# Kernel tuning notes

Hardware: AMD Instinct MI355X
Metric: run time of the kernel (lower is better)

The kernel has to match this reference:

```python
import jax, jax.numpy as jnp
import numpy as np

N = 6144          # number_of_nodes
E = 196608        # random edges (self-loops appended in reference, as add_self_loops does)
L_GAT = 10        # GAT num_layers
NEG_SLOPE = 0.2   # GATConv leaky_relu slope


def setup_inputs() -> dict:
    key = jax.random.key(0)
    ks = jax.random.split(key, 27)
    g = lambda i, shape, s=0.3: jax.random.normal(ks[i], shape, jnp.float32) * s
    return {
        "x": jax.random.normal(ks[0], (N, 3), jnp.float32),
        "mask": jax.random.uniform(ks[1], (N,), dtype=jnp.float32),
        "edge_index": jax.random.randint(ks[2], (2, E), 0, N),
        # 10-layer GAT (heads=1): per-layer lin weight, att_src, att_dst, bias
        "gat_W": g(3, (L_GAT, 3, 3)), "gat_asrc": g(4, (L_GAT, 3)),
        "gat_adst": g(5, (L_GAT, 3)), "gat_b": g(6, (L_GAT, 3), 0.1),
        # nn.MultiheadAttention(embed_dim=3, num_heads=3)
        "mha_in_w": g(7, (9, 3)), "mha_in_b": g(8, (9,), 0.1),
        "mha_out_w": g(9, (3, 3)), "mha_out_b": g(10, (3,), 0.1),
        # TransformerConv(3, 3, heads=1)
        "tc_Wq": g(11, (3, 3)), "tc_bq": g(12, (3,), 0.1),
        "tc_Wk": g(13, (3, 3)), "tc_bk": g(14, (3,), 0.1),
        "tc_Wv": g(15, (3, 3)), "tc_bv": g(16, (3,), 0.1),
        "tc_Wskip": g(17, (3, 3)), "tc_bskip": g(18, (3,), 0.1),
        # actor MLP: Linear(3N,16) -> ReLU -> Linear(16,32) -> ReLU -> Linear(32,N)
        "mlp_W1": g(19, (3 * N, 16), 0.02), "mlp_b1": g(20, (16,), 0.1),
        "mlp_W2": g(21, (16, 32), 0.2), "mlp_b2": g(22, (32,), 0.1),
        "mlp_W3": g(23, (32, N), 0.2), "mlp_b3": jnp.zeros((N,), jnp.float32),
        # critic Linear(1,1)
        "critic_W": g(24, (1, 1)), "critic_b": g(25, (1,), 0.1),
    }


def _seg_softmax(e, seg, n):
    # numerically-stable softmax grouped by destination node
    m = jax.lax.stop_gradient(jax.ops.segment_max(e, seg, num_segments=n))
    w = jnp.exp(e - m[seg])
    z = jax.ops.segment_sum(w, seg, num_segments=n)
    return w / (z[seg] + 1e-16)


def reference(x, mask, edge_index, gat_W, gat_asrc, gat_adst, gat_b,
              mha_in_w, mha_in_b, mha_out_w, mha_out_b,
              tc_Wq, tc_bq, tc_Wk, tc_bk, tc_Wv, tc_bv, tc_Wskip, tc_bskip,
              mlp_W1, mlp_b1, mlp_W2, mlp_b2, mlp_W3, mlp_b3,
              critic_W, critic_b):
    n = x.shape[0]
    loops = jnp.arange(n)
    src = jnp.concatenate([edge_index[0], loops])  # add_self_loops
    dst = jnp.concatenate([edge_index[1], loops])

    # ---- 10-layer GAT (heads=1, ReLU between layers) ----
    h = x
    for l in range(L_GAT):
        xp = h @ gat_W[l]                                   # [N,3]
        e = jax.nn.leaky_relu(xp[src] @ gat_asrc[l] + xp[dst] @ gat_adst[l], NEG_SLOPE)
        alpha = _seg_softmax(e, dst, n)
        h_new = jax.ops.segment_sum(alpha[:, None] * xp[src], dst, num_segments=n) + gat_b[l]
        h = jax.nn.relu(h_new) if l < L_GAT - 1 else h_new

    # ---- MultiheadAttention(embed_dim=3, num_heads=3 => head_dim=1), history = [h] ----
    qkv = h @ mha_in_w.T + mha_in_b                         # [N,9]
    q, k, v = qkv[:, 0:3], qkv[:, 3:6], qkv[:, 6:9]
    scores = jnp.einsum('nh,mh->hnm', q, k)                 # head_dim=1 -> scale = 1
    attn = jax.nn.softmax(scores, axis=-1)                  # [3,N,N] -- dominant memory
    o = jnp.einsum('hnm,mh->nh', attn, v)                   # [N,3]
    h2 = o @ mha_out_w.T + mha_out_b

    # ---- TransformerConv(3, 3, heads=1) ----
    q2 = h2 @ tc_Wq + tc_bq
    k2 = h2 @ tc_Wk + tc_bk
    v2 = h2 @ tc_Wv + tc_bv
    logit = (q2[dst] * k2[src]).sum(-1) * (1.0 / np.sqrt(3.0))
    alpha2 = _seg_softmax(logit, dst, n)
    agg = jax.ops.segment_sum(alpha2[:, None] * v2[src], dst, num_segments=n)
    h3 = agg + h2 @ tc_Wskip + tc_bskip                     # root_weight skip

    # ---- actor MLP over flattened node features ----
    flat = h3.reshape(-1)                                   # [3N]
    a1 = jax.nn.relu(flat @ mlp_W1 + mlp_b1)
    a2 = jax.nn.relu(a1 @ mlp_W2 + mlp_b2)
    results = (a2 @ mlp_W3 + mlp_b3)[:, None]               # [N,1]

    new_results = results[:, 0] * mask
    value = jnp.mean(results @ critic_W + critic_b)
    return new_results, value
```

## Files before the change

kernel.cpp:

```cpp
#include <hip/hip_runtime.h>

#define N 6144
#define E 196608
#define EN (E + N)
#define LGAT 10
#define HBLK 198
#define GBLK 384
#define MCH 192

typedef unsigned int u32;

__device__ __forceinline__ u32 f2key(float f) {
    u32 u = __float_as_uint(f);
    return (u & 0x80000000u) ? ~u : (u | 0x80000000u);
}
__device__ __forceinline__ float key2f(u32 k) {
    u32 u = (k & 0x80000000u) ? (k & 0x7FFFFFFFu) : ~k;
    return __uint_as_float(u);
}
__device__ __forceinline__ float aload_f(const float* p2) {
    return __hip_atomic_load(p2, __ATOMIC_RELAXED, __HIP_MEMORY_SCOPE_AGENT);
}
__device__ __forceinline__ u32 aload_u(const u32* p2) {
    return __hip_atomic_load(p2, __ATOMIC_RELAXED, __HIP_MEMORY_SCOPE_AGENT);
}

struct P {
    const float *x, *mask, *gat_W, *gat_asrc, *gat_adst, *gat_b;
    const float *in_w, *in_b, *out_w, *out_b;
    const float *Wq, *bq, *Wk, *bk, *Wv, *bv, *Wsk, *bsk;
    const float *W1, *b1, *W2, *b2, *W3, *b3, *cW, *cb;
    const int *src, *dst;
    float4 *nodeA, *nodeB;
    float *sdstA, *sdstB;
    float *qkv, *q2, *h2, *h3, *part;
    float4 *kv2;
    float *a1pre, *a2buf, *sumres;
    u32 *deg, *offs, *cursor, *kmaxk, *kmink;
    u32 *kmaxk2, *kmink2;
    u32 *ssmaxk;
    u32 *ctr;
    int *ssorted;
    float *out;
};

__global__ void k_init(P p) {
    int t = blockIdx.x * 256 + threadIdx.x;
    p.deg[t] = 0u;
    if (t < 16) p.a1pre[t] = 0.f;
    else if (t == 16) p.sumres[0] = 0.f;
    else if (t >= 32 && t < 35) { p.kmaxk[t - 32] = 0u; p.kmink[t - 32] = 0xFFFFFFFFu; }
    else if (t >= 35 && t < 38) { p.kmaxk2[t - 35] = 0u; p.kmink2[t - 35] = 0xFFFFFFFFu; }
    else if (t >= 48 && t < 48 + LGAT) p.ssmaxk[t - 48] = 0u;
    else if (t >= 64 && t < 72) p.ctr[t - 64] = 0u;
}

__global__ void k_hist(P p) {
    __shared__ u32 spart[256];
    __shared__ bool last;
    int t = blockIdx.x * 256 + threadIdx.x;
    #pragma unroll
    for (int k = 0; k < 4; ++k) {
        int e = t + k * (HBLK * 256);
        int d = (e < E) ? p.dst[e] : (e - E);
        atomicAdd(&p.deg[d], 1u);
    }
    __syncthreads();
    if (threadIdx.x == 0) {
        __threadfence();
        last = (atomicAdd(&p.ctr[0], 1u) == HBLK - 1);
    }
    __syncthreads();
    if (!last) return;
    int tid = threadIdx.x;
    u32 loc[24];
    u32 sum = 0;
    #pragma unroll
    for (int i = 0; i < 24; ++i) { loc[i] = sum; sum += aload_u(&p.deg[tid * 24 + i]); }
    spart[tid] = sum;
    __syncthreads();
    for (int o = 1; o < 256; o <<= 1) {
        u32 v = (tid >= o) ? spart[tid - o] : 0u;
        __syncthreads();
        spart[tid] += v;
        __syncthreads();
    }
    u32 base = (tid == 0) ? 0u : spart[tid - 1];
    #pragma unroll
    for (int i = 0; i < 24; ++i) {
        u32 off = base + loc[i];
        p.offs[tid * 24 + i] = off;
        p.cursor[tid * 24 + i] = off;
    }
    if (tid == 255) p.offs[N] = spart[255];
}

__global__ void k_scatter(P p) {
    int t = blockIdx.x * 256 + threadIdx.x;
    #pragma unroll
    for (int k = 0; k < 4; ++k) {
        int e = t + k * (HBLK * 256);
        int s = (e < E) ? p.src[e] : (e - E);
        int d = (e < E) ? p.dst[e] : (e - E);
        u32 pos = atomicAdd(&p.cursor[d], 1u);
        p.ssorted[pos] = s;
    }
    if (t < N) {
        float h0 = p.x[t * 3 + 0], h1 = p.x[t * 3 + 1], h2 = p.x[t * 3 + 2];
        const float* W = p.gat_W;
        float xp0 = h0 * W[0] + h1 * W[3] + h2 * W[6];
        float xp1 = h0 * W[1] + h1 * W[4] + h2 * W[7];
        float xp2 = h0 * W[2] + h1 * W[5] + h2 * W[8];
        float ss = xp0 * p.gat_asrc[0] + xp1 * p.gat_asrc[1] + xp2 * p.gat_asrc[2];
        p.nodeA[t] = make_float4(xp0, xp1, xp2, ss);
        p.sdstA[t] = xp0 * p.gat_adst[0] + xp1 * p.gat_adst[1] + xp2 * p.gat_adst[2];
        float m = ss;
        #pragma unroll
        for (int o = 32; o; o >>= 1) m = fmaxf(m, __shfl_xor(m, o));
        if ((threadIdx.x & 63) == 0) atomicMax(&p.ssmaxk[0], f2key(m));
    }
}

__global__ __launch_bounds__(256) void k_gat(P p, const float4* __restrict__ nin,
                                             const float* __restrict__ sdin,
                                             float4* __restrict__ nout,
                                             float* __restrict__ sdout, int l) {
    __shared__ float ssh[16];
    __shared__ float kksh[16][3];
    int gid = blockIdx.x * 256 + threadIdx.x;
    int d = gid >> 4;
    int lane = gid & 15;
    int tid = threadIdx.x;
    u32 beg = p.offs[d], end = p.offs[d + 1];
    float sd = sdin[d];
    float vb = key2f(p.ssmaxk[l]) + sd;
    float M = (vb >= 0.f) ? vb : 0.2f * vb;
    float sz = 0.f, s0 = 0.f, s1 = 0.f, s2 = 0.f;
    for (u32 i = beg + lane; i < end; i += 16) {
        float4 r = nin[p.ssorted[i]];
        float v = r.w + sd;
        v = (v >= 0.f) ? v : 0.2f * v;
        float w = __expf(v - M);
        sz += w; s0 += w * r.x; s1 += w * r.y; s2 += w * r.z;
    }
    #pragma unroll
    for (int o = 1; o < 16; o <<= 1) {
        sz += __shfl_xor(sz, o);
        s0 += __shfl_xor(s0, o);
        s1 += __shfl_xor(s1, o);
        s2 += __shfl_xor(s2, o);
    }
    if (lane == 0) {
        float z = sz + 1e-16f;
        float o0 = s0 / z + p.gat_b[l * 3 + 0];
        float o1 = s1 / z + p.gat_b[l * 3 + 1];
        float o2 = s2 / z + p.gat_b[l * 3 + 2];
        if (l < LGAT - 1) {
            o0 = fmaxf(o0, 0.f); o1 = fmaxf(o1, 0.f); o2 = fmaxf(o2, 0.f);
            const float* W = p.gat_W + (l + 1) * 9;
            float xp0 = o0 * W[0] + o1 * W[3] + o2 * W[6];
            float xp1 = o0 * W[1] + o1 * W[4] + o2 * W[7];
            float xp2 = o0 * W[2] + o1 * W[5] + o2 * W[8];
            const float* as = p.gat_asrc + (l + 1) * 3;
            const float* ad = p.gat_adst + (l + 1) * 3;
            float ss = xp0 * as[0] + xp1 * as[1] + xp2 * as[2];
            nout[d] = make_float4(xp0, xp1, xp2, ss);
            sdout[d] = xp0 * ad[0] + xp1 * ad[1] + xp2 * ad[2];
            ssh[tid >> 4] = ss;
        } else {
            float kk[9];
            #pragma unroll
            for (int j = 0; j < 9; ++j) {
                kk[j] = o0 * p.in_w[j * 3 + 0] + o1 * p.in_w[j * 3 + 1] +
                        o2 * p.in_w[j * 3 + 2] + p.in_b[j];
                p.qkv[d * 9 + j] = kk[j];
            }
            kksh[tid >> 4][0] = kk[3];
            kksh[tid >> 4][1] = kk[4];
            kksh[tid >> 4][2] = kk[5];
        }
    }
    __syncthreads();
    if (l < LGAT - 1) {
        if (tid == 0) {
            float m = ssh[0];
            #pragma unroll
            for (int j = 1; j < 16; ++j) m = fmaxf(m, ssh[j]);
            atomicMax(&p.ssmaxk[l + 1], f2key(m));
        }
    } else {
        if (tid < 3) {
            float mx = -1e30f, mn = 1e30f;
            #pragma unroll
            for (int g = 0; g < 16; ++g) {
                mx = fmaxf(mx, kksh[g][tid]);
                mn = fminf(mn, kksh[g][tid]);
            }
            atomicMax(&p.kmaxk[tid], f2key(mx));
            atomicMin(&p.kmink[tid], f2key(mn));
        }
    }
}

__global__ void k_att_partial(P p) {
    __shared__ float4 kvA[MCH];
    __shared__ float2 kvB[MCH];
    int tid = threadIdx.x;
    int chunk = blockIdx.y;
    int mbase = chunk * MCH;
    for (int mm = tid; mm < MCH; mm += 256) {
        const float* qk = p.qkv + (size_t)(mbase + mm) * 9;
        kvA[mm] = make_float4(qk[3], qk[4], qk[5], qk[6]);
        kvB[mm] = make_float2(qk[7], qk[8]);
    }
    __syncthreads();
    int n = blockIdx.x * 256 + tid;
    float q0 = p.qkv[n * 9 + 0], q1 = p.qkv[n * 9 + 1], q2 = p.qkv[n * 9 + 2];
    float kmx0 = key2f(p.kmaxk[0]), kmx1 = key2f(p.kmaxk[1]), kmx2 = key2f(p.kmaxk[2]);
    float kmn0 = key2f(p.kmink[0]), kmn1 = key2f(p.kmink[1]), kmn2 = key2f(p.kmink[2]);
    float M0 = (q0 >= 0.f) ? q0 * kmx0 : q0 * kmn0;
    float M1 = (q1 >= 0.f) ? q1 * kmx1 : q1 * kmn1;
    float M2 = (q2 >= 0.f) ? q2 * kmx2 : q2 * kmn2;
    float num0 = 0, den0 = 0, num1 = 0, den1 = 0, num2 = 0, den2 = 0;
    #pragma unroll 4
    for (int mm = 0; mm < MCH; ++mm) {
        float4 a = kvA[mm];
        float2 b = kvB[mm];
        float t0 = __expf(q0 * a.x - M0); den0 += t0; num0 += t0 * a.w;
        float t1 = __expf(q1 * a.y - M1); den1 += t1; num1 += t1 * b.x;
        float t2 = __expf(q2 * a.z - M2); den2 += t2; num2 += t2 * b.y;
    }
    float* pp = p.part + (size_t)chunk * 6 * N + n;
    pp[0] = num0; pp[N] = den0; pp[2 * N] = num1;
    pp[3 * N] = den1; pp[4 * N] = num2; pp[5 * N] = den2;
}

__global__ void k_att_reduce(P p) {
    int n = blockIdx.x * 256 + threadIdx.x;
    float num[3] = {0.f, 0.f, 0.f}, den[3] = {0.f, 0.f, 0.f};
    for (int c = 0; c < 32; ++c) {
        const float* pp = p.part + (size_t)c * 6 * N + n;
        #pragma unroll
        for (int hh = 0; hh < 3; ++hh) {
            num[hh] += pp[hh * 2 * N];
            den[hh] += pp[(hh * 2 + 1) * N];
        }
    }
    float o[3];
    #pragma unroll
    for (int hh = 0; hh < 3; ++hh) o[hh] = num[hh] / den[hh];
    float h2v[3];
    #pragma unroll
    for (int c = 0; c < 3; ++c) {
        h2v[c] = p.out_b[c] + o[0] * p.out_w[c * 3 + 0] +
                 o[1] * p.out_w[c * 3 + 1] + o[2] * p.out_w[c * 3 + 2];
        p.h2[n * 3 + c] = h2v[c];
    }
    float q2v[3], k2v[3], v2v[3];
    #pragma unroll
    for (int c = 0; c < 3; ++c) {
        q2v[c] = p.bq[c] + h2v[0] * p.Wq[c] + h2v[1] * p.Wq[3 + c] + h2v[2] * p.Wq[6 + c];
        k2v[c] = p.bk[c] + h2v[0] * p.Wk[c] + h2v[1] * p.Wk[3 + c] + h2v[2] * p.Wk[6 + c];
        v2v[c] = p.bv[c] + h2v[0] * p.Wv[c] + h2v[1] * p.Wv[3 + c] + h2v[2] * p.Wv[6 + c];
        p.q2[n * 3 + c] = q2v[c];
    }
    p.kv2[n * 2 + 0] = make_float4(k2v[0], k2v[1], k2v[2], v2v[0]);
    p.kv2[n * 2 + 1] = make_float4(v2v[1], v2v[2], 0.f, 0.f);
    #pragma unroll
    for (int hh = 0; hh < 3; ++hh) {
        float mx = k2v[hh], mn = k2v[hh];
        #pragma unroll
        for (int o2 = 32; o2; o2 >>= 1) {
            mx = fmaxf(mx, __shfl_xor(mx, o2));
            mn = fminf(mn, __shfl_xor(mn, o2));
        }
        if ((threadIdx.x & 63) == 0) {
            atomicMax(&p.kmaxk2[hh], f2key(mx));
            atomicMin(&p.kmink2[hh], f2key(mn));
        }
    }
}

__global__ __launch_bounds__(256) void k_tc_edge(P p) {
    int gid = blockIdx.x * 256 + threadIdx.x;
    int d = gid >> 4;
    int lane = gid & 15;
    u32 beg = p.offs[d], end = p.offs[d + 1];
    float q0 = p.q2[d * 3 + 0], q1 = p.q2[d * 3 + 1], q2 = p.q2[d * 3 + 2];
    const float RS3 = 0.57735026919f;
    float kx0 = key2f(p.kmaxk2[0]), kx1 = key2f(p.kmaxk2[1]), kx2 = key2f(p.kmaxk2[2]);
    float kn0 = key2f(p.kmink2[0]), kn1 = key2f(p.kmink2[1]), kn2 = key2f(p.kmink2[2]);
    float M = ((q0 >= 0.f ? q0 * kx0 : q0 * kn0) +
               (q1 >= 0.f ? q1 * kx1 : q1 * kn1) +
               (q2 >= 0.f ? q2 * kx2 : q2 * kn2)) * RS3;
    float sz = 0.f, s0 = 0.f, s1 = 0.f, s2 = 0.f;
    for (u32 i = beg + lane; i < end; i += 16) {
        int s = p.ssorted[i];
        float4 ka = p.kv2[s * 2];
        float4 kb = p.kv2[s * 2 + 1];
        float lg = (q0 * ka.x + q1 * ka.y + q2 * ka.z) * RS3;
        float w = __expf(lg - M);
        sz += w;
        s0 += w * ka.w; s1 += w * kb.x; s2 += w * kb.y;
    }
    #pragma unroll
    for (int o = 1; o < 16; o <<= 1) {
        sz += __shfl_xor(sz, o);
        s0 += __shfl_xor(s0, o);
        s1 += __shfl_xor(s1, o);
        s2 += __shfl_xor(s2, o);
    }
    if (lane == 0) {
        float z = sz + 1e-16f;
        float h0 = p.h2[d * 3 + 0], h1 = p.h2[d * 3 + 1], h2 = p.h2[d * 3 + 2];
        float agg[3] = {s0 / z, s1 / z, s2 / z};
        #pragma unroll
        for (int c = 0; c < 3; ++c) {
            p.h3[d * 3 + c] = agg[c] + p.bsk[c] +
                h0 * p.Wsk[c] + h1 * p.Wsk[3 + c] + h2 * p.Wsk[6 + c];
        }
    }
}

__global__ void k_mlp1(P p) {
    __shared__ float red[64];
    __shared__ bool last;
    int t = blockIdx.x * 256 + threadIdx.x;
    int j = t & 15;
    int g = t >> 4;
    float acc = 0.f;
    #pragma unroll
    for (int k = 0; k < 16; ++k) {
        int r = g + k * 1152;
        acc += p.h3[r] * p.W1[r * 16 + j];
    }
    acc += __shfl_xor(acc, 16);
    acc += __shfl_xor(acc, 32);
    int tid = threadIdx.x;
    if ((tid & 63) < 16) red[(tid >> 6) * 16 + j] = acc;
    __syncthreads();
    if (tid < 16) {
        float s = red[tid] + red[16 + tid] + red[32 + tid] + red[48 + tid];
        atomicAdd(&p.a1pre[tid], s);
    }
    __syncthreads();
    if (tid == 0) {
        __threadfence();
        last = (atomicAdd(&p.ctr[2], 1u) == 71u);
    }
    __syncthreads();
    if (!last) return;
    if (tid < 32) {
        float acc2 = p.b2[tid];
        #pragma unroll
        for (int i = 0; i < 16; ++i) {
            float a1 = fmaxf(aload_f(&p.a1pre[i]) + p.b1[i], 0.f);
            acc2 += a1 * p.W2[i * 32 + tid];
        }
        p.a2buf[tid] = fmaxf(acc2, 0.f);
    }
}

__global__ void k_mlp3(P p) {
    __shared__ float a2[32];
    __shared__ bool last;
    int tid = threadIdx.x;
    if (tid < 32) a2[tid] = p.a2buf[tid];
    __syncthreads();
    int n = blockIdx.x * 256 + tid;
    float acc = p.b3[n];
    #pragma unroll
    for (int j = 0; j < 32; ++j) acc += a2[j] * p.W3[(size_t)j * N + n];
    p.out[n] = acc * p.mask[n];
    float s = acc;
    #pragma unroll
    for (int o = 32; o; o >>= 1) s += __shfl_xor(s, o);
    if ((tid & 63) == 0) atomicAdd(p.sumres, s);
    __syncthreads();
    if (tid == 0) {
        __threadfence();
        last = (atomicAdd(&p.ctr[3], 1u) == 23u);
    }
    __syncthreads();
    if (last && tid == 0) {
        float sr = aload_f(p.sumres);
        p.out[N] = p.cW[0] * (sr / (float)N) + p.cb[0];
    }
}

extern "C" void kernel_launch(void* const* d_in, const int* in_sizes, int n_in,
                              void* d_out, int out_size, void* d_ws, size_t ws_size,
                              hipStream_t stream) {
    P p;
    p.x      = (const float*)d_in[0];
    p.mask   = (const float*)d_in[1];
    const int* ei = (const int*)d_in[2];
    p.src = ei; p.dst = ei + E;
    p.gat_W  = (const float*)d_in[3];
    p.gat_asrc = (const float*)d_in[4];
    p.gat_adst = (const float*)d_in[5];
    p.gat_b  = (const float*)d_in[6];
    p.in_w   = (const float*)d_in[7];
    p.in_b   = (const float*)d_in[8];
    p.out_w  = (const float*)d_in[9];
    p.out_b  = (const float*)d_in[10];
    p.Wq = (const float*)d_in[11]; p.bq = (const float*)d_in[12];
    p.Wk = (const float*)d_in[13]; p.bk = (const float*)d_in[14];
    p.Wv = (const float*)d_in[15]; p.bv = (const float*)d_in[16];
    p.Wsk = (const float*)d_in[17]; p.bsk = (const float*)d_in[18];
    p.W1 = (const float*)d_in[19]; p.b1 = (const float*)d_in[20];
    p.W2 = (const float*)d_in[21]; p.b2 = (const float*)d_in[22];
    p.W3 = (const float*)d_in[23]; p.b3 = (const float*)d_in[24];
    p.cW = (const float*)d_in[25]; p.cb = (const float*)d_in[26];

    float* ws = (float*)d_ws;
    p.nodeA   = (float4*)(ws + 0);
    p.nodeB   = (float4*)(ws + 24576);
    p.sdstA   = ws + 49152;
    p.sdstB   = ws + 55296;
    p.qkv     = ws + 61440;
    p.q2      = ws + 116736;
    p.kv2     = (float4*)(ws + 135168);
    p.h2      = ws + 184320;
    p.h3      = ws + 202752;
    p.part    = ws + 221184;
    p.a1pre   = ws + 1400832;
    p.a2buf   = ws + 1400848;
    p.sumres  = ws + 1400880;
    p.kmaxk   = (u32*)(ws + 1400884);
    p.kmink   = (u32*)(ws + 1400887);
    p.deg     = (u32*)(ws + 1400890);
    p.offs    = (u32*)(ws + 1407034);
    p.cursor  = (u32*)(ws + 1413179);
    p.ssorted = (int*)(ws + 1419323);
    p.kmaxk2  = (u32*)(ws + 1622075);
    p.kmink2  = (u32*)(ws + 1622078);
    p.ssmaxk  = (u32*)(ws + 1622081);
    p.ctr     = (u32*)(ws + 1622091);
    p.out     = (float*)d_out;

    k_init<<<24, 256, 0, stream>>>(p);
    k_hist<<<HBLK, 256, 0, stream>>>(p);
    k_scatter<<<HBLK, 256, 0, stream>>>(p);
    for (int l = 0; l < LGAT; ++l) {
        const float4* nin = (l & 1) ? p.nodeB : p.nodeA;
        const float*  sdin = (l & 1) ? p.sdstB : p.sdstA;
        float4* nout = (l & 1) ? p.nodeA : p.nodeB;
        float*  sdout = (l & 1) ? p.sdstA : p.sdstB;
        k_gat<<<GBLK, 256, 0, stream>>>(p, nin, sdin, nout, sdout, l);
    }
    k_att_partial<<<dim3(24, 32), 256, 0, stream>>>(p);
    k_att_reduce<<<24, 256, 0, stream>>>(p);
    k_tc_edge<<<GBLK, 256, 0, stream>>>(p);
    k_mlp1<<<72, 256, 0, stream>>>(p);
    k_mlp3<<<24, 256, 0, stream>>>(p);
}
```

Before: 290.7 us.

## Fuse MLP first layer into TransformerConv edge kernel and widen per-node lanes

The first actor MLP layer is folded into the TransformerConv aggregation kernel. Each block keeps its 8 nodes' h3 values in shared memory and accumulates its 24 rows of W1 into padded atomic slots, so the h3 buffer and the separate mlp1 launch go away. The GAT and TC kernels now give 32 lanes per destination node instead of 16, which doubles the block count. This trades more atomics on the a1 accumulators (768 blocks) and more idle lanes for nodes with few edges against one fewer launch and one fewer global round trip.

```diff
diff --git a/kernel.cpp b/kernel.cpp
--- a/kernel.cpp
+++ b/kernel.cpp
@@ -5,7 +5,7 @@
 #define EN (E + N)
 #define LGAT 10
 #define HBLK 198
-#define GBLK 384
+#define GBLK 768
 #define MCH 192
 
 typedef unsigned int u32;
@@ -33,9 +33,10 @@
     const int *src, *dst;
     float4 *nodeA, *nodeB;
     float *sdstA, *sdstB;
-    float *qkv, *q2, *h2, *h3, *part;
+    float *qkv, *q2, *h2, *part;
     float4 *kv2;
-    float *a1pre, *a2buf, *sumres;
+    float *a1pre;
+    float *a2buf, *sumres;
     u32 *deg, *offs, *cursor, *kmaxk, *kmink;
     u32 *kmaxk2, *kmink2;
     u32 *ssmaxk;
@@ -47,12 +48,12 @@
 __global__ void k_init(P p) {
     int t = blockIdx.x * 256 + threadIdx.x;
     p.deg[t] = 0u;
-    if (t < 16) p.a1pre[t] = 0.f;
-    else if (t == 16) p.sumres[0] = 0.f;
-    else if (t >= 32 && t < 35) { p.kmaxk[t - 32] = 0u; p.kmink[t - 32] = 0xFFFFFFFFu; }
-    else if (t >= 35 && t < 38) { p.kmaxk2[t - 35] = 0u; p.kmink2[t - 35] = 0xFFFFFFFFu; }
-    else if (t >= 48 && t < 48 + LGAT) p.ssmaxk[t - 48] = 0u;
-    else if (t >= 64 && t < 72) p.ctr[t - 64] = 0u;
+    if (t < 256) p.a1pre[t] = 0.f;
+    else if (t == 256) p.sumres[0] = 0.f;
+    else if (t >= 257 && t < 260) { p.kmaxk[t - 257] = 0u; p.kmink[t - 257] = 0xFFFFFFFFu; }
+    else if (t >= 260 && t < 263) { p.kmaxk2[t - 260] = 0u; p.kmink2[t - 260] = 0xFFFFFFFFu; }
+    else if (t >= 272 && t < 272 + LGAT) p.ssmaxk[t - 272] = 0u;
+    else if (t >= 288 && t < 296) p.ctr[t - 288] = 0u;
 }
 
 __global__ void k_hist(P p) {
@@ -125,18 +126,18 @@
                                              const float* __restrict__ sdin,
                                              float4* __restrict__ nout,
                                              float* __restrict__ sdout, int l) {
-    __shared__ float ssh[16];
-    __shared__ float kksh[16][3];
+    __shared__ float ssh[8];
+    __shared__ float kksh[8][3];
     int gid = blockIdx.x * 256 + threadIdx.x;
-    int d = gid >> 4;
-    int lane = gid & 15;
+    int d = gid >> 5;
+    int lane = gid & 31;
     int tid = threadIdx.x;
     u32 beg = p.offs[d], end = p.offs[d + 1];
     float sd = sdin[d];
     float vb = key2f(p.ssmaxk[l]) + sd;
     float M = (vb >= 0.f) ? vb : 0.2f * vb;
     float sz = 0.f, s0 = 0.f, s1 = 0.f, s2 = 0.f;
-    for (u32 i = beg + lane; i < end; i += 16) {
+    for (u32 i = beg + lane; i < end; i += 32) {
         float4 r = nin[p.ssorted[i]];
         float v = r.w + sd;
         v = (v >= 0.f) ? v : 0.2f * v;
@@ -144,7 +145,7 @@
         sz += w; s0 += w * r.x; s1 += w * r.y; s2 += w * r.z;
     }
     #pragma unroll
-    for (int o = 1; o < 16; o <<= 1) {
+    for (int o = 1; o < 32; o <<= 1) {
         sz += __shfl_xor(sz, o);
         s0 += __shfl_xor(s0, o);
         s1 += __shfl_xor(s1, o);
@@ -166,7 +167,7 @@
             float ss = xp0 * as[0] + xp1 * as[1] + xp2 * as[2];
             nout[d] = make_float4(xp0, xp1, xp2, ss);
             sdout[d] = xp0 * ad[0] + xp1 * ad[1] + xp2 * ad[2];
-            ssh[tid >> 4] = ss;
+            ssh[tid >> 5] = ss;
         } else {
             float kk[9];
             #pragma unroll
@@ -175,9 +176,9 @@
                         o2 * p.in_w[j * 3 + 2] + p.in_b[j];
                 p.qkv[d * 9 + j] = kk[j];
             }
-            kksh[tid >> 4][0] = kk[3];
-            kksh[tid >> 4][1] = kk[4];
-            kksh[tid >> 4][2] = kk[5];
+            kksh[tid >> 5][0] = kk[3];
+            kksh[tid >> 5][1] = kk[4];
+            kksh[tid >> 5][2] = kk[5];
         }
     }
     __syncthreads();
@@ -185,14 +186,14 @@
         if (tid == 0) {
             float m = ssh[0];
             #pragma unroll
-            for (int j = 1; j < 16; ++j) m = fmaxf(m, ssh[j]);
+            for (int j = 1; j < 8; ++j) m = fmaxf(m, ssh[j]);
             atomicMax(&p.ssmaxk[l + 1], f2key(m));
         }
     } else {
         if (tid < 3) {
             float mx = -1e30f, mn = 1e30f;
             #pragma unroll
-            for (int g = 0; g < 16; ++g) {
+            for (int g = 0; g < 8; ++g) {
                 mx = fmaxf(mx, kksh[g][tid]);
                 mn = fminf(mn, kksh[g][tid]);
             }
@@ -238,6 +239,7 @@
 __global__ void k_att_reduce(P p) {
     int n = blockIdx.x * 256 + threadIdx.x;
     float num[3] = {0.f, 0.f, 0.f}, den[3] = {0.f, 0.f, 0.f};
+    #pragma unroll 4
     for (int c = 0; c < 32; ++c) {
         const float* pp = p.part + (size_t)c * 6 * N + n;
         #pragma unroll
@@ -282,9 +284,12 @@
 }
 
 __global__ __launch_bounds__(256) void k_tc_edge(P p) {
+    __shared__ float h3sh[24];
+    __shared__ bool last;
     int gid = blockIdx.x * 256 + threadIdx.x;
-    int d = gid >> 4;
-    int lane = gid & 15;
+    int d = gid >> 5;
+    int lane = gid & 31;
+    int tid = threadIdx.x;
     u32 beg = p.offs[d], end = p.offs[d + 1];
     float q0 = p.q2[d * 3 + 0], q1 = p.q2[d * 3 + 1], q2 = p.q2[d * 3 + 2];
     const float RS3 = 0.57735026919f;
@@ -294,7 +299,7 @@
                (q1 >= 0.f ? q1 * kx1 : q1 * kn1) +
                (q2 >= 0.f ? q2 * kx2 : q2 * kn2)) * RS3;
     float sz = 0.f, s0 = 0.f, s1 = 0.f, s2 = 0.f;
-    for (u32 i = beg + lane; i < end; i += 16) {
+    for (u32 i = beg + lane; i < end; i += 32) {
         int s = p.ssorted[i];
         float4 ka = p.kv2[s * 2];
         float4 kb = p.kv2[s * 2 + 1];
@@ -304,7 +309,7 @@
         s0 += w * ka.w; s1 += w * kb.x; s2 += w * kb.y;
     }
     #pragma unroll
-    for (int o = 1; o < 16; o <<= 1) {
+    for (int o = 1; o < 32; o <<= 1) {
         sz += __shfl_xor(sz, o);
         s0 += __shfl_xor(s0, o);
         s1 += __shfl_xor(s1, o);
@@ -314,39 +319,26 @@
         float z = sz + 1e-16f;
         float h0 = p.h2[d * 3 + 0], h1 = p.h2[d * 3 + 1], h2 = p.h2[d * 3 + 2];
         float agg[3] = {s0 / z, s1 / z, s2 / z};
+        int g = tid >> 5;
         #pragma unroll
         for (int c = 0; c < 3; ++c) {
-            p.h3[d * 3 + c] = agg[c] + p.bsk[c] +
+            h3sh[g * 3 + c] = agg[c] + p.bsk[c] +
                 h0 * p.Wsk[c] + h1 * p.Wsk[3 + c] + h2 * p.Wsk[6 + c];
         }
     }
-}
-
-__global__ void k_mlp1(P p) {
-    __shared__ float red[64];
-    __shared__ bool last;
-    int t = blockIdx.x * 256 + threadIdx.x;
-    int j = t & 15;
-    int g = t >> 4;
-    float acc = 0.f;
-    #pragma unroll
-    for (int k = 0; k < 16; ++k) {
-        int r = g + k * 1152;
-        acc += p.h3[r] * p.W1[r * 16 + j];
-    }
-    acc += __shfl_xor(acc, 16);
-    acc += __shfl_xor(acc, 32);
-    int tid = threadIdx.x;
-    if ((tid & 63) < 16) red[(tid >> 6) * 16 + j] = acc;
     __syncthreads();
     if (tid < 16) {
-        float s = red[tid] + red[16 + tid] + red[32 + tid] + red[48 + tid];
-        atomicAdd(&p.a1pre[tid], s);
+        int rbase = blockIdx.x * 24;
+        float acc = 0.f;
+        #pragma unroll
+        for (int r = 0; r < 24; ++r)
+            acc += h3sh[r] * p.W1[(size_t)(rbase + r) * 16 + tid];
+        atomicAdd(&p.a1pre[tid * 16], acc);
     }
     __syncthreads();
     if (tid == 0) {
         __threadfence();
-        last = (atomicAdd(&p.ctr[2], 1u) == 71u);
+        last = (atomicAdd(&p.ctr[2], 1u) == GBLK - 1);
     }
     __syncthreads();
     if (!last) return;
@@ -354,7 +346,7 @@
         float acc2 = p.b2[tid];
         #pragma unroll
         for (int i = 0; i < 16; ++i) {
-            float a1 = fmaxf(aload_f(&p.a1pre[i]) + p.b1[i], 0.f);
+            float a1 = fmaxf(aload_f(&p.a1pre[i * 16]) + p.b1[i], 0.f);
             acc2 += a1 * p.W2[i * 32 + tid];
         }
         p.a2buf[tid] = fmaxf(acc2, 0.f);
@@ -422,21 +414,20 @@
     p.q2      = ws + 116736;
     p.kv2     = (float4*)(ws + 135168);
     p.h2      = ws + 184320;
-    p.h3      = ws + 202752;
-    p.part    = ws + 221184;
-    p.a1pre   = ws + 1400832;
-    p.a2buf   = ws + 1400848;
-    p.sumres  = ws + 1400880;
-    p.kmaxk   = (u32*)(ws + 1400884);
-    p.kmink   = (u32*)(ws + 1400887);
-    p.deg     = (u32*)(ws + 1400890);
-    p.offs    = (u32*)(ws + 1407034);
-    p.cursor  = (u32*)(ws + 1413179);
-    p.ssorted = (int*)(ws + 1419323);
-    p.kmaxk2  = (u32*)(ws + 1622075);
-    p.kmink2  = (u32*)(ws + 1622078);
-    p.ssmaxk  = (u32*)(ws + 1622081);
-    p.ctr     = (u32*)(ws + 1622091);
+    p.part    = ws + 202752;
+    p.a1pre   = ws + 1382400;
+    p.a2buf   = ws + 1382656;
+    p.sumres  = ws + 1382688;
+    p.kmaxk   = (u32*)(ws + 1382689);
+    p.kmink   = (u32*)(ws + 1382692);
+    p.deg     = (u32*)(ws + 1382695);
+    p.offs    = (u32*)(ws + 1388839);
+    p.cursor  = (u32*)(ws + 1394984);
+    p.ssorted = (int*)(ws + 1401128);
+    p.kmaxk2  = (u32*)(ws + 1603880);
+    p.kmink2  = (u32*)(ws + 1603883);
+    p.ssmaxk  = (u32*)(ws + 1603886);
+    p.ctr     = (u32*)(ws + 1603896);
     p.out     = (float*)d_out;
 
     k_init<<<24, 256, 0, stream>>>(p);
@@ -452,6 +443,5 @@
     k_att_partial<<<dim3(24, 32), 256, 0, stream>>>(p);
     k_att_reduce<<<24, 256, 0, stream>>>(p);
     k_tc_edge<<<GBLK, 256, 0, stream>>>(p);
-    k_mlp1<<<72, 256, 0, stream>>>(p);
     k_mlp3<<<24, 256, 0, stream>>>(p);
 }
```

Result: slower. 359.2 us (+23.5%).
